# Kernel tuning notes

Hardware: AMD Instinct MI355X
Metric: run time of the kernel (lower is better)

The kernel has to match this reference:

```python
import jax, jax.numpy as jnp
import numpy as np

N_NODES = 100000
N_EDGES = 1600000
F_IN = 128
F_HID = 128


def _sage_mean(x, src, dst, W_self, W_neigh, b, n_nodes):
    # DGL SAGEConv('mean'): out = x @ W_self + mean_{u in in-nbrs(v)} x_u @ W_neigh + b
    # nodes with zero in-degree get a zero neighbor aggregate (DGL copy_u/mean semantics)
    deg = jax.ops.segment_sum(jnp.ones_like(dst, dtype=x.dtype), dst, num_segments=n_nodes)
    agg = jax.ops.segment_sum(x[src], dst, num_segments=n_nodes)  # [N, F] irregular scatter-add
    agg = agg / jnp.maximum(deg, 1.0)[:, None]
    return x @ W_self + agg @ W_neigh + b


def setup_inputs() -> dict:
    key = jax.random.key(0)
    ks = jax.random.split(key, 8)
    s_in = 1.0 / np.sqrt(F_IN)
    s_hid = 1.0 / np.sqrt(F_HID)
    return {
        "x": jax.random.normal(ks[0], (N_NODES, F_IN), dtype=jnp.float32),
        "W_self1": jax.random.normal(ks[1], (F_IN, F_HID), dtype=jnp.float32) * s_in,
        "W_neigh1": jax.random.normal(ks[2], (F_IN, F_HID), dtype=jnp.float32) * s_in,
        "b1": jnp.zeros((F_HID,), dtype=jnp.float32),
        "W_self2": jax.random.normal(ks[3], (F_HID, F_HID), dtype=jnp.float32) * s_hid,
        "W_neigh2": jax.random.normal(ks[4], (F_HID, F_HID), dtype=jnp.float32) * s_hid,
        "b2": jnp.zeros((F_HID,), dtype=jnp.float32),
        "src": jax.random.randint(ks[5], (N_EDGES,), 0, N_NODES, dtype=jnp.int32),
        "dst": jax.random.randint(ks[6], (N_EDGES,), 0, N_NODES, dtype=jnp.int32),
    }


def reference(x, W_self1, W_neigh1, b1, W_self2, W_neigh2, b2, src, dst):
    n = x.shape[0]
    h = _sage_mean(x, src, dst, W_self1, W_neigh1, b1, n)
    h = jax.nn.relu(h)
    h = _sage_mean(h, src, dst, W_self2, W_neigh2, b2, n)
    return h
```

## Files before the change

### kernel.cpp

```cpp
#include <hip/hip_runtime.h>
#include <hip/hip_bf16.h>
#include <stdint.h>

#define F 128
#define CHUNK 4096
#define NSH 8
#define NMSK 255
#define BCAP 4608

typedef float f32x4 __attribute__((ext_vector_type(4)));
typedef float f32x2 __attribute__((ext_vector_type(2)));
typedef short bf16x8 __attribute__((ext_vector_type(8)));

__device__ __forceinline__ unsigned short f2bf(float f) {
    unsigned u = __float_as_uint(f);
    unsigned r = 0x7fffu + ((u >> 16) & 1u);
    return (unsigned short)((u + r) >> 16);
}
__device__ __forceinline__ unsigned pk_bf16(float lo, float hi) {
    unsigned r;
    asm("v_cvt_pk_bf16_f32 %0, %1, %2" : "=v"(r) : "v"(lo), "v"(hi));
    return r;
}

__global__ __launch_bounds__(256) void convert_kernel(const float* __restrict__ in,
                                                      unsigned short* __restrict__ outb,
                                                      unsigned char* __restrict__ out8, long n) {
    long i = ((long)blockIdx.x * 256 + threadIdx.x) * 8;
    if (i >= n) return;
    float4 a = *(const float4*)(in + i);
    float4 b = *(const float4*)(in + i + 4);
    uint4 o;
    o.x = pk_bf16(a.x, a.y);
    o.y = pk_bf16(a.z, a.w);
    o.z = pk_bf16(b.x, b.y);
    o.w = pk_bf16(b.z, b.w);
    *(uint4*)(outb + i) = o;
    int p0 = __builtin_amdgcn_cvt_pk_fp8_f32(a.x, a.y, 0, false);
    p0 = __builtin_amdgcn_cvt_pk_fp8_f32(a.z, a.w, p0, true);
    int p1 = __builtin_amdgcn_cvt_pk_fp8_f32(b.x, b.y, 0, false);
    p1 = __builtin_amdgcn_cvt_pk_fp8_f32(b.z, b.w, p1, true);
    uint2 q;
    q.x = (unsigned)p0;
    q.y = (unsigned)p1;
    *(uint2*)(out8 + i) = q;
}

__global__ __launch_bounds__(256) void pack_w_kernel(const float* __restrict__ Ws,
                                                     const float* __restrict__ Wn,
                                                     unsigned short* __restrict__ Wp) {
    for (int i = blockIdx.x * 256 + threadIdx.x; i < 32768; i += gridDim.x * 256) {
        int j = i & 7;
        int g = (i >> 3) & 3;
        int c = (i >> 5) & 127;
        int s = (i >> 12) & 7;
        int k = (s & 3) * 32 + g * 8 + j;
        const float* W = (s < 4) ? Ws : Wn;
        Wp[i] = f2bf(W[k * F + c]);
    }
}

__global__ __launch_bounds__(512) void init_cursor_kernel(int* __restrict__ gcursor,
                                                          unsigned* __restrict__ dummy_row,
                                                          int nbk) {
    int t = blockIdx.x * 512 + threadIdx.x;
    if (t < nbk) gcursor[t] = t * BCAP;
    if (blockIdx.x == 0 && threadIdx.x < F / 4) dummy_row[threadIdx.x] = 0u;
}

__global__ __launch_bounds__(1024) void scatter1_kernel(const int* __restrict__ src,
                                                        const int* __restrict__ dst,
                                                        int* __restrict__ gcursor,
                                                        unsigned* __restrict__ packed,
                                                        int nE, int nbk) {
    __shared__ int hist[512];
    __shared__ int curs[512];
    int t = threadIdx.x;
    for (int i = t; i < nbk; i += 1024) hist[i] = 0;
    __syncthreads();
    int base = blockIdx.x * CHUNK;
    int end = min(base + CHUNK, nE);
    for (int e = base + t; e < end; e += 1024)
        atomicAdd(&hist[dst[e] >> NSH], 1);
    __syncthreads();
    for (int i = t; i < nbk; i += 1024)
        if (hist[i]) curs[i] = atomicAdd(&gcursor[i], hist[i]);
    __syncthreads();
    for (int e = base + t; e < end; e += 1024) {
        int d = dst[e];
        int b = d >> NSH;
        int pos = atomicAdd(&curs[b], 1);
        packed[pos] = (unsigned)src[e] | ((unsigned)(d & NMSK) << 24);
    }
}

__global__ __launch_bounds__(1024) void csr2_kernel(const unsigned* __restrict__ packed,
                                                    const int* __restrict__ gcursor,
                                                    int* __restrict__ esrc,
                                                    int* __restrict__ offsets,
                                                    int* __restrict__ deg, int nN) {
    __shared__ int cnt[256];
    __shared__ int curs[256];
    __shared__ int wsum[4];
    int b = blockIdx.x;
    int estart = b * BCAP;
    int eend = gcursor[b];
    int t = threadIdx.x;
    if (t < 256) cnt[t] = 0;
    __syncthreads();
    for (int e = estart + t; e < eend; e += 1024)
        atomicAdd(&cnt[packed[e] >> 24], 1);
    __syncthreads();
    int lane = t & 63, w = t >> 6;
    int v = (t < 256) ? cnt[t] : 0;
    int incl = v;
    #pragma unroll
    for (int off = 1; off < 64; off <<= 1) {
        int u = __shfl_up(incl, off, 64);
        if (lane >= off) incl += u;
    }
    if (t < 256 && lane == 63) wsum[w] = incl;
    __syncthreads();
    if (t < 256) {
        int pre = 0;
        #pragma unroll
        for (int i = 0; i < 3; ++i)
            if (i < w) pre += wsum[i];
        int ex = pre + incl - v;
        curs[t] = ex;
        int id = b * 256 + t;
        if (id < nN) {
            offsets[id] = estart + ex;
            deg[id] = v;
        }
    }
    __syncthreads();
    for (int e = estart + t; e < eend; e += 1024) {
        unsigned u = packed[e];
        int d = u >> 24;
        int pos = atomicAdd(&curs[d], 1);
        esrc[estart + pos] = (int)(u & 0x00FFFFFFu);
    }
}

__global__ __launch_bounds__(256) void aggregate_kernel(const unsigned char* __restrict__ f8,
                                                        const int* __restrict__ esrc,
                                                        const int* __restrict__ offsets,
                                                        const int* __restrict__ deg,
                                                        unsigned short* __restrict__ agg, int nN) {
    int node = blockIdx.x * 32 + (threadIdx.x >> 3);
    int s = threadIdx.x & 7;
    if (node >= nN) return;
    int beg = offsets[node];
    int dg = deg[node];
    int mx = dg;
    mx = max(mx, __shfl_xor(mx, 8, 64));
    mx = max(mx, __shfl_xor(mx, 16, 64));
    mx = max(mx, __shfl_xor(mx, 32, 64));
    f32x2 a[8];
    #pragma unroll
    for (int i = 0; i < 8; ++i) a[i] = (f32x2)0.f;
    #pragma unroll 2
    for (int i = 0; i < mx; ++i) {
        int srcn = esrc[beg + i];
        srcn = (i < dg) ? srcn : nN;
        const unsigned char* rp = f8 + (size_t)srcn * F + s * 16;
        uint4 v = *(const uint4*)rp;
        a[0] += __builtin_amdgcn_cvt_pk_f32_fp8(v.x, false);
        a[1] += __builtin_amdgcn_cvt_pk_f32_fp8(v.x, true);
        a[2] += __builtin_amdgcn_cvt_pk_f32_fp8(v.y, false);
        a[3] += __builtin_amdgcn_cvt_pk_f32_fp8(v.y, true);
        a[4] += __builtin_amdgcn_cvt_pk_f32_fp8(v.z, false);
        a[5] += __builtin_amdgcn_cvt_pk_f32_fp8(v.z, true);
        a[6] += __builtin_amdgcn_cvt_pk_f32_fp8(v.w, false);
        a[7] += __builtin_amdgcn_cvt_pk_f32_fp8(v.w, true);
    }
    float inv = 1.0f / (float)(dg > 0 ? dg : 1);
    uint4 o0, o1;
    o0.x = pk_bf16(a[0].x * inv, a[0].y * inv);
    o0.y = pk_bf16(a[1].x * inv, a[1].y * inv);
    o0.z = pk_bf16(a[2].x * inv, a[2].y * inv);
    o0.w = pk_bf16(a[3].x * inv, a[3].y * inv);
    o1.x = pk_bf16(a[4].x * inv, a[4].y * inv);
    o1.y = pk_bf16(a[5].x * inv, a[5].y * inv);
    o1.z = pk_bf16(a[6].x * inv, a[6].y * inv);
    o1.w = pk_bf16(a[7].x * inv, a[7].y * inv);
    uint4* dp = (uint4*)(agg + (size_t)node * F + s * 16);
    dp[0] = o0;
    dp[1] = o1;
}

#define LDA 136
__global__ __launch_bounds__(256) void gemm_mfma_kernel(const unsigned short* __restrict__ self,
                                                        const unsigned short* __restrict__ agg,
                                                        const unsigned short* __restrict__ Wp,
                                                        const float* __restrict__ bias,
                                                        void* __restrict__ out,
                                                        unsigned char* __restrict__ out8,
                                                        int relu, int out_bf16, int nN) {
    __shared__ __align__(16) unsigned short sA[64][LDA];
    __shared__ __align__(16) unsigned short sG[64][LDA];
    int t = threadIdx.x;
    int row0 = blockIdx.x * 64;

    #pragma unroll
    for (int it = 0; it < 4; ++it) {
        int chunk = it * 256 + t;
        int r = chunk >> 4;
        int c8 = (chunk & 15) << 3;
        int rg = row0 + r;
        if (rg >= nN) rg = nN - 1;
        *(uint4*)&sA[r][c8] = *(const uint4*)(self + (size_t)rg * F + c8);
        *(uint4*)&sG[r][c8] = *(const uint4*)(agg + (size_t)rg * F + c8);
    }
    __syncthreads();

    int wid = t >> 6;
    int lane = t & 63;
    int l15 = lane & 15;
    int g = lane >> 4;

    f32x4 acc[4][2];
    #pragma unroll
    for (int m = 0; m < 4; ++m)
        #pragma unroll
        for (int n = 0; n < 2; ++n) acc[m][n] = (f32x4)0.f;

    #pragma unroll
    for (int s = 0; s < 8; ++s) {
        const unsigned short (*sIn)[LDA] = (s < 4) ? sA : sG;
        int klocal = (s & 3) * 32 + g * 8;
        bf16x8 a[4], b[2];
        #pragma unroll
        for (int m = 0; m < 4; ++m)
            a[m] = *(const bf16x8*)&sIn[m * 16 + l15][klocal];
        #pragma unroll
        for (int n = 0; n < 2; ++n) {
            int c = wid * 32 + n * 16 + l15;
            b[n] = *(const bf16x8*)(Wp + (((size_t)s * 128 + c) * 4 + g) * 8);
        }
        #pragma unroll
        for (int m = 0; m < 4; ++m)
            #pragma unroll
            for (int n = 0; n < 2; ++n)
                acc[m][n] = __builtin_amdgcn_mfma_f32_16x16x32_bf16(a[m], b[n], acc[m][n], 0, 0, 0);
    }

    #pragma unroll
    for (int n = 0; n < 2; ++n) {
        int c = wid * 32 + n * 16 + l15;
        float bv = bias[c];
        #pragma unroll
        for (int m = 0; m < 4; ++m) {
            #pragma unroll
            for (int r = 0; r < 4; ++r) {
                int row = row0 + m * 16 + g * 4 + r;
                if (row >= nN) continue;
                float v = acc[m][n][r] + bv;
                if (relu) v = fmaxf(v, 0.f);
                if (out_bf16)
                    ((unsigned short*)out)[(size_t)row * F + c] = f2bf(v);
                else
                    ((float*)out)[(size_t)row * F + c] = v;
                if (out8)
                    out8[(size_t)row * F + c] =
                        (unsigned char)(__builtin_amdgcn_cvt_pk_fp8_f32(v, v, 0, false) & 0xff);
            }
        }
    }
}

extern "C" void kernel_launch(void* const* d_in, const int* in_sizes, int n_in,
                              void* d_out, int out_size, void* d_ws, size_t ws_size,
                              hipStream_t stream) {
    const float* x   = (const float*)d_in[0];
    const float* Ws1 = (const float*)d_in[1];
    const float* Wn1 = (const float*)d_in[2];
    const float* b1  = (const float*)d_in[3];
    const float* Ws2 = (const float*)d_in[4];
    const float* Wn2 = (const float*)d_in[5];
    const float* b2  = (const float*)d_in[6];
    const int* src   = (const int*)d_in[7];
    const int* dst   = (const int*)d_in[8];

    int nN = in_sizes[0] / F;
    int nE = in_sizes[7];
    int nbk = (nN + NMSK) >> NSH;
    int nbe = (nE + CHUNK - 1) / CHUNK;

    char* p = (char*)d_ws;
    int* gcursor = (int*)p;  p += (size_t)nbk * 4;
    int* offsets = (int*)p;  p += (size_t)nN * 4;
    int* deg = (int*)p;      p += (size_t)nN * 4;
    unsigned* packed = (unsigned*)p; p += (size_t)nbk * BCAP * 4;
    int* esrc = (int*)p;     p += (size_t)nbk * BCAP * 4;
    p = (char*)(((uintptr_t)p + 255) & ~(uintptr_t)255);
    unsigned short* Wp1 = (unsigned short*)p; p += 32768 * 2;
    unsigned short* Wp2 = (unsigned short*)p; p += 32768 * 2;
    unsigned short* xb = (unsigned short*)p; p += (size_t)nN * F * 2;
    unsigned short* hb = (unsigned short*)p; p += (size_t)nN * F * 2;
    unsigned short* agg1 = (unsigned short*)d_out;
    unsigned char* q8 = (unsigned char*)d_out + (size_t)nN * F * 2;

    long nElem = (long)nN * F;
    convert_kernel<<<(int)((nElem / 8 + 255) / 256), 256, 0, stream>>>(x, xb, q8, nElem);
    pack_w_kernel<<<16, 256, 0, stream>>>(Ws1, Wn1, Wp1);
    pack_w_kernel<<<16, 256, 0, stream>>>(Ws2, Wn2, Wp2);

    init_cursor_kernel<<<(nbk + 511) / 512, 512, 0, stream>>>(
        gcursor, (unsigned*)(q8 + (size_t)nN * F), nbk);
    scatter1_kernel<<<nbe, 1024, 0, stream>>>(src, dst, gcursor, packed, nE, nbk);
    csr2_kernel<<<nbk, 1024, 0, stream>>>(packed, gcursor, esrc, offsets, deg, nN);

    int ablocks = (nN + 31) / 32;
    int gblocks = (nN + 63) / 64;

    aggregate_kernel<<<ablocks, 256, 0, stream>>>(q8, esrc, offsets, deg, agg1, nN);
    gemm_mfma_kernel<<<gblocks, 256, 0, stream>>>(xb, agg1, Wp1, b1, hb, q8, 1, 1, nN);
    aggregate_kernel<<<ablocks, 256, 0, stream>>>(q8, esrc, offsets, deg, xb, nN);
    gemm_mfma_kernel<<<gblocks, 256, 0, stream>>>(hb, xb, Wp2, b2, d_out, nullptr, 0, 0, nN);
}
```

Baseline: 185.6 us.

## Sort nodes by degree within buckets and fuse init/pack kernel launches

The CSR build now also counting-sorts nodes by in-degree within each 256-node bucket and emits an order array. The aggregate kernel walks nodes in that order, so the 8-lane groups sharing a wavefront have similar degrees and waste fewer padded iterations. Cursor initialisation is folded into the convert kernel, and the two weight-pack launches are merged into one to cut launch overhead. In exchange, the aggregate output rows and offsets are accessed in permuted order, which costs an extra indirection.

```diff
diff --git a/kernel.cpp b/kernel.cpp
--- a/kernel.cpp
+++ b/kernel.cpp
@@ -25,7 +25,15 @@
 
 __global__ __launch_bounds__(256) void convert_kernel(const float* __restrict__ in,
                                                       unsigned short* __restrict__ outb,
-                                                      unsigned char* __restrict__ out8, long n) {
+                                                      unsigned char* __restrict__ out8,
+                                                      int* __restrict__ gcursor,
+                                                      unsigned* __restrict__ dummy_row,
+                                                      int nbk, long n) {
+    if (blockIdx.x < 2) {
+        int ii = blockIdx.x * 256 + threadIdx.x;
+        if (ii < nbk) gcursor[ii] = ii * BCAP;
+        if (ii < F / 4) dummy_row[ii] = 0u;
+    }
     long i = ((long)blockIdx.x * 256 + threadIdx.x) * 8;
     if (i >= n) return;
     float4 a = *(const float4*)(in + i);
@@ -46,10 +54,17 @@
     *(uint2*)(out8 + i) = q;
 }
 
-__global__ __launch_bounds__(256) void pack_w_kernel(const float* __restrict__ Ws,
-                                                     const float* __restrict__ Wn,
-                                                     unsigned short* __restrict__ Wp) {
-    for (int i = blockIdx.x * 256 + threadIdx.x; i < 32768; i += gridDim.x * 256) {
+__global__ __launch_bounds__(256) void pack_w_kernel(const float* __restrict__ Ws1,
+                                                     const float* __restrict__ Wn1,
+                                                     const float* __restrict__ Ws2,
+                                                     const float* __restrict__ Wn2,
+                                                     unsigned short* __restrict__ Wp1,
+                                                     unsigned short* __restrict__ Wp2) {
+    int half = blockIdx.x >> 4;
+    const float* Ws = half ? Ws2 : Ws1;
+    const float* Wn = half ? Wn2 : Wn1;
+    unsigned short* Wp = half ? Wp2 : Wp1;
+    for (int i = (blockIdx.x & 15) * 256 + threadIdx.x; i < 32768; i += 16 * 256) {
         int j = i & 7;
         int g = (i >> 3) & 3;
         int c = (i >> 5) & 127;
@@ -58,14 +73,6 @@
         const float* W = (s < 4) ? Ws : Wn;
         Wp[i] = f2bf(W[k * F + c]);
     }
-}
-
-__global__ __launch_bounds__(512) void init_cursor_kernel(int* __restrict__ gcursor,
-                                                          unsigned* __restrict__ dummy_row,
-                                                          int nbk) {
-    int t = blockIdx.x * 512 + threadIdx.x;
-    if (t < nbk) gcursor[t] = t * BCAP;
-    if (blockIdx.x == 0 && threadIdx.x < F / 4) dummy_row[threadIdx.x] = 0u;
 }
 
 __global__ __launch_bounds__(1024) void scatter1_kernel(const int* __restrict__ src,
@@ -98,21 +105,26 @@
                                                     const int* __restrict__ gcursor,
                                                     int* __restrict__ esrc,
                                                     int* __restrict__ offsets,
-                                                    int* __restrict__ deg, int nN) {
+                                                    int* __restrict__ deg,
+                                                    int* __restrict__ order, int nN) {
     __shared__ int cnt[256];
     __shared__ int curs[256];
     __shared__ int wsum[4];
+    __shared__ int dhoff[64];
     int b = blockIdx.x;
     int estart = b * BCAP;
     int eend = gcursor[b];
     int t = threadIdx.x;
     if (t < 256) cnt[t] = 0;
+    if (t >= 256 && t < 320) dhoff[t - 256] = 0;
     __syncthreads();
     for (int e = estart + t; e < eend; e += 1024)
         atomicAdd(&cnt[packed[e] >> 24], 1);
     __syncthreads();
     int lane = t & 63, w = t >> 6;
     int v = (t < 256) ? cnt[t] : 0;
+    int id = b * 256 + t;
+    if (t < 256 && id < nN) atomicAdd(&dhoff[min(v, 63)], 1);
     int incl = v;
     #pragma unroll
     for (int off = 1; off < 64; off <<= 1) {
@@ -120,6 +132,17 @@
         if (lane >= off) incl += u;
     }
     if (t < 256 && lane == 63) wsum[w] = incl;
+    __syncthreads();
+    if (t < 64) {
+        int bv = dhoff[t];
+        int binc = bv;
+        #pragma unroll
+        for (int off = 1; off < 64; off <<= 1) {
+            int u = __shfl_up(binc, off, 64);
+            if (t >= off) binc += u;
+        }
+        dhoff[t] = binc - bv;
+    }
     __syncthreads();
     if (t < 256) {
         int pre = 0;
@@ -128,10 +151,11 @@
             if (i < w) pre += wsum[i];
         int ex = pre + incl - v;
         curs[t] = ex;
-        int id = b * 256 + t;
         if (id < nN) {
             offsets[id] = estart + ex;
             deg[id] = v;
+            int rank = atomicAdd(&dhoff[min(v, 63)], 1);
+            order[b * 256 + rank] = id;
         }
     }
     __syncthreads();
@@ -147,10 +171,12 @@
                                                         const int* __restrict__ esrc,
                                                         const int* __restrict__ offsets,
                                                         const int* __restrict__ deg,
+                                                        const int* __restrict__ order,
                                                         unsigned short* __restrict__ agg, int nN) {
-    int node = blockIdx.x * 32 + (threadIdx.x >> 3);
+    int gid = blockIdx.x * 32 + (threadIdx.x >> 3);
     int s = threadIdx.x & 7;
-    if (node >= nN) return;
+    if (gid >= nN) return;
+    int node = order[gid];
     int beg = offsets[node];
     int dg = deg[node];
     int mx = dg;
@@ -292,6 +318,7 @@
     int* gcursor = (int*)p;  p += (size_t)nbk * 4;
     int* offsets = (int*)p;  p += (size_t)nN * 4;
     int* deg = (int*)p;      p += (size_t)nN * 4;
+    int* order = (int*)p;    p += (size_t)nbk * 256 * 4;
     unsigned* packed = (unsigned*)p; p += (size_t)nbk * BCAP * 4;
     int* esrc = (int*)p;     p += (size_t)nbk * BCAP * 4;
     p = (char*)(((uintptr_t)p + 255) & ~(uintptr_t)255);
@@ -303,20 +330,18 @@
     unsigned char* q8 = (unsigned char*)d_out + (size_t)nN * F * 2;
 
     long nElem = (long)nN * F;
-    convert_kernel<<<(int)((nElem / 8 + 255) / 256), 256, 0, stream>>>(x, xb, q8, nElem);
-    pack_w_kernel<<<16, 256, 0, stream>>>(Ws1, Wn1, Wp1);
-    pack_w_kernel<<<16, 256, 0, stream>>>(Ws2, Wn2, Wp2);
-
-    init_cursor_kernel<<<(nbk + 511) / 512, 512, 0, stream>>>(
-        gcursor, (unsigned*)(q8 + (size_t)nN * F), nbk);
+    convert_kernel<<<(int)((nElem / 8 + 255) / 256), 256, 0, stream>>>(
+        x, xb, q8, gcursor, (unsigned*)(q8 + (size_t)nN * F), nbk, nElem);
+    pack_w_kernel<<<32, 256, 0, stream>>>(Ws1, Wn1, Ws2, Wn2, Wp1, Wp2);
+
     scatter1_kernel<<<nbe, 1024, 0, stream>>>(src, dst, gcursor, packed, nE, nbk);
-    csr2_kernel<<<nbk, 1024, 0, stream>>>(packed, gcursor, esrc, offsets, deg, nN);
+    csr2_kernel<<<nbk, 1024, 0, stream>>>(packed, gcursor, esrc, offsets, deg, order, nN);
 
     int ablocks = (nN + 31) / 32;
     int gblocks = (nN + 63) / 64;
 
-    aggregate_kernel<<<ablocks, 256, 0, stream>>>(q8, esrc, offsets, deg, agg1, nN);
+    aggregate_kernel<<<ablocks, 256, 0, stream>>>(q8, esrc, offsets, deg, order, agg1, nN);
     gemm_mfma_kernel<<<gblocks, 256, 0, stream>>>(xb, agg1, Wp1, b1, hb, q8, 1, 1, nN);
-    aggregate_kernel<<<ablocks, 256, 0, stream>>>(q8, esrc, offsets, deg, xb, nN);
+    aggregate_kernel<<<ablocks, 256, 0, stream>>>(q8, esrc, offsets, deg, order, xb, nN);
     gemm_mfma_kernel<<<gblocks, 256, 0, stream>>>(hb, xb, Wp2, b2, d_out, nullptr, 0, 0, nN);
 }
```

New measurement: 196.7 us. 6.0% more time.
